# Performance work log

Hardware: AMD Instinct MI355X
Metric: run time of the kernel (lower is better)

Reference implementation:

```python
import jax, jax.numpy as jnp
import numpy as np

COORD_DIM = 2
ENTITY_DIM = 1024
FIELD_DIM = 512
INPUT_DIM = 512
NUM_ENTITIES = 512
FIELD_RESOLUTION = 10000  # grid_size = 100


def _gelu(x):
    return jax.nn.gelu(x, approximate=False)  # torch nn.GELU default (erf)


def setup_inputs() -> dict:
    key = jax.random.key(0)
    ks = jax.random.split(key, 9)
    std = 0.02  # matches _init_parameters
    B, S = 8, 4096
    x = jax.random.normal(ks[0], (B, S, INPUT_DIM), dtype=jnp.float32)
    # DensityField: density_projection = Linear(D,F) GELU Linear(F,F) GELU; coordinate_generator = Linear(F,2)
    W1 = jax.random.normal(ks[1], (INPUT_DIM, FIELD_DIM), jnp.float32) * std
    b1 = jnp.zeros((FIELD_DIM,), jnp.float32)
    W2 = jax.random.normal(ks[2], (FIELD_DIM, FIELD_DIM), jnp.float32) * std
    b2 = jnp.zeros((FIELD_DIM,), jnp.float32)
    Wc = jax.random.normal(ks[3], (FIELD_DIM, COORD_DIM), jnp.float32) * std
    bc = jnp.zeros((COORD_DIM,), jnp.float32)
    # entity_mapper: Linear(F+2, F) GELU Linear(F, E+2+1)
    We1 = jax.random.normal(ks[4], (FIELD_DIM + COORD_DIM, FIELD_DIM), jnp.float32) * std
    be1 = jnp.zeros((FIELD_DIM,), jnp.float32)
    We2 = jax.random.normal(ks[5], (FIELD_DIM, ENTITY_DIM + COORD_DIM + 1), jnp.float32) * std
    be2 = jnp.zeros((ENTITY_DIM + COORD_DIM + 1,), jnp.float32)
    # output_projection: Linear(E, 2E) GELU Linear(2E, D)
    Wo1 = jax.random.normal(ks[6], (ENTITY_DIM, 2 * ENTITY_DIM), jnp.float32) * std
    bo1 = jnp.zeros((2 * ENTITY_DIM,), jnp.float32)
    Wo2 = jax.random.normal(ks[7], (2 * ENTITY_DIM, INPUT_DIM), jnp.float32) * std
    bo2 = jnp.zeros((INPUT_DIM,), jnp.float32)
    return dict(x=x, W1=W1, b1=b1, W2=W2, b2=b2, Wc=Wc, bc=bc,
                We1=We1, be1=be1, We2=We2, be2=be2,
                Wo1=Wo1, bo1=bo1, Wo2=Wo2, bo2=bo2)


def _forward(x, W1, b1, W2, b2, Wc, bc, We1, be1, We2, be2, Wo1, bo1, Wo2, bo2):
    # --- DensityField ---
    df = _gelu(_gelu(x @ W1 + b1) @ W2 + b2)          # [B,S,F]
    coords = df @ Wc + bc                              # [B,S,2]
    # --- ContinuousEntityExtractor ---
    field_input = jnp.concatenate([coords, df], axis=-1)          # [B,S,2+F]
    ef = _gelu(field_input @ We1 + be1) @ We2 + be2                # [B,S,E+3]
    importance = jnp.linalg.norm(ef, axis=-1)                      # [B,S]
    _, top_idx = jax.lax.top_k(importance, NUM_ENTITIES)           # [B,Ne]
    sel = jnp.take_along_axis(ef, top_idx[..., None], axis=1)     # [B,Ne,E+3]
    positions = sel[..., :COORD_DIM]                               # [B,Ne,2]
    states = sel[..., COORD_DIM:COORD_DIM + ENTITY_DIM]            # [B,Ne,E]
    # --- ContinuousOutputGenerator ---
    proj = _gelu(states @ Wo1 + bo1) @ Wo2 + bo2                   # [B,Ne,D]
    grid_size = int(FIELD_RESOLUTION ** 0.5)
    g = jnp.linspace(-1.0, 1.0, grid_size)
    gx, gy = jnp.meshgrid(g, g, indexing='ij')
    grid = jnp.stack([gx.ravel(), gy.ravel()], axis=-1)            # [G2,2]
    # squared euclidean distances via expansion (torch: cdist then **2)
    g2 = jnp.sum(grid * grid, axis=-1)                             # [G2]
    p2 = jnp.sum(positions * positions, axis=-1)                   # [B,Ne]
    gp = jnp.einsum('gc,bnc->bgn', grid, positions)                # [B,G2,Ne]
    sq = g2[None, :, None] + p2[:, None, :] - 2.0 * gp             # [B,G2,Ne]
    attn = jnp.exp(-sq / 0.1)
    attn = attn / (attn.sum(axis=-1, keepdims=True) + 1e-8)
    out = jnp.einsum('bgn,bnd->bgd', attn, proj)                   # [B,G2,D]
    return out


def reference(x, W1, b1, W2, b2, Wc, bc, We1, be1, We2, be2, Wo1, bo1, Wo2, bo2):
    return _forward(x, W1, b1, W2, b2, Wc, bc, We1, be1, We2, be2, Wo1, bo1, Wo2, bo2)
```

## Files before the change

kernel.cpp:

```cpp
#include <hip/hip_runtime.h>
#include <hip/hip_bf16.h>
#include <math.h>


typedef __attribute__((ext_vector_type(8))) short bf16x8;
typedef __attribute__((ext_vector_type(4))) float f32x4;

__device__ __forceinline__ float gelu_exact(float x) {
    return 0.5f * x * (1.0f + erff(x * 0.7071067811865476f));
}

__device__ __forceinline__ void async_copy16(const void* g, void* l) {
    __builtin_amdgcn_global_load_lds(
        (const __attribute__((address_space(1))) unsigned int*)g,
        (__attribute__((address_space(3))) unsigned int*)l, 16, 0, 0);
}

__global__ __launch_bounds__(256) void split_kernel(
    const float* __restrict__ in,
    __hip_bfloat16* __restrict__ hi, __hip_bfloat16* __restrict__ lo)
{
    const int i4 = blockIdx.x * 256 + threadIdx.x;
    const float4 v = ((const float4*)in)[i4];
    __hip_bfloat16 h0 = __float2bfloat16(v.x);
    __hip_bfloat16 h1 = __float2bfloat16(v.y);
    __hip_bfloat16 h2 = __float2bfloat16(v.z);
    __hip_bfloat16 h3 = __float2bfloat16(v.w);
    __hip_bfloat16 l0 = __float2bfloat16(v.x - __bfloat162float(h0));
    __hip_bfloat16 l1 = __float2bfloat16(v.y - __bfloat162float(h1));
    __hip_bfloat16 l2 = __float2bfloat16(v.z - __bfloat162float(h2));
    __hip_bfloat16 l3 = __float2bfloat16(v.w - __bfloat162float(h3));
    union { __hip_bfloat16 h[4]; short4 s; } uh, ul;
    uh.h[0] = h0; uh.h[1] = h1; uh.h[2] = h2; uh.h[3] = h3;
    ul.h[0] = l0; ul.h[1] = l1; ul.h[2] = l2; ul.h[3] = l3;
    ((short4*)hi)[i4] = uh.s;
    ((short4*)lo)[i4] = ul.s;
}

__global__ __launch_bounds__(256) void transpose_split_kernel(
    const float* __restrict__ in,
    __hip_bfloat16* __restrict__ outH, __hip_bfloat16* __restrict__ outL,
    int K, int N)
{
    __shared__ float tile[32][33];
    const int k0 = blockIdx.y * 32, n0 = blockIdx.x * 32;
    const int t = threadIdx.x;
    const int lr = t >> 5, lc = t & 31;
    #pragma unroll
    for (int p = 0; p < 4; p++) {
        const int r = p * 8 + lr;
        const int n = n0 + lc;
        tile[r][lc] = (n < N) ? in[(size_t)(k0 + r) * N + n] : 0.f;
    }
    __syncthreads();
    #pragma unroll
    for (int p = 0; p < 4; p++) {
        const int r = p * 8 + lr;
        const float v = tile[lc][r];
        const __hip_bfloat16 h = __float2bfloat16(v);
        const __hip_bfloat16 l = __float2bfloat16(v - __bfloat162float(h));
        outH[(size_t)(n0 + r) * K + k0 + lc] = h;
        outL[(size_t)(n0 + r) * K + k0 + lc] = l;
    }
}

__global__ __launch_bounds__(256) void init_kernel(
    float* __restrict__ IMP, float* __restrict__ CRD,
    const float* __restrict__ bc)
{
    const int t = blockIdx.x * 256 + threadIdx.x;
    IMP[t] = 0.f;
    ((float2*)CRD)[t] = make_float2(bc[0], bc[1]);
}

template<bool GELU, bool RANK2, bool SPLIT, bool FUSEC, bool FUSEI>
__device__ __forceinline__ void gemm3k_body(
    const __hip_bfloat16* __restrict__ Ahi, const __hip_bfloat16* __restrict__ Alo,
    const __hip_bfloat16* __restrict__ Bhi, const __hip_bfloat16* __restrict__ Blo,
    const float* __restrict__ bias,
    float* __restrict__ Cf, int ldc,
    __hip_bfloat16* __restrict__ Chi, __hip_bfloat16* __restrict__ Clo,
    int N,
    const float* __restrict__ A2, const float* __restrict__ W2r,
    float* __restrict__ CRD, const float* __restrict__ Wc,
    float* __restrict__ IMP)
{
    __shared__ __align__(16) __hip_bfloat16 AsH[128][32];
    __shared__ __align__(16) __hip_bfloat16 AsL[128][32];
    __shared__ __align__(16) __hip_bfloat16 BsH[128][32];
    __shared__ __align__(16) __hip_bfloat16 BsL[128][32];
    const int t = threadIdx.x;
    const int wave = t >> 6, lane = t & 63;
    const int wave_m = wave >> 1, wave_n = wave & 1;
    const int fr = lane & 15, quad = lane >> 4;
    const int m0 = blockIdx.y * 128;
    const int n0 = blockIdx.x * 128;
    const int srow = lane >> 2;
    const int skc  = (lane & 3) * 8;

    f32x4 acc[4][4] = {};

    for (int k0 = 0; k0 < 512; k0 += 32) {
        #pragma unroll
        for (int s = 0; s < 2; s++) {
            const int seg = wave * 2 + s;
            const int row = seg * 16 + srow;
            const size_t ao = (size_t)(m0 + row) * 512 + k0 + skc;
            const size_t bo = (size_t)(n0 + row) * 512 + k0 + skc;
            async_copy16(Ahi + ao, &AsH[seg * 16][0]);
            async_copy16(Alo + ao, &AsL[seg * 16][0]);
            async_copy16(Bhi + bo, &BsH[seg * 16][0]);
            async_copy16(Blo + bo, &BsL[seg * 16][0]);
        }
        __syncthreads();
        bf16x8 ah[4], al[4], bh[4], bl[4];
        #pragma unroll
        for (int i = 0; i < 4; i++) {
            ah[i] = *(const bf16x8*)&AsH[wave_m * 64 + i * 16 + fr][quad * 8];
            al[i] = *(const bf16x8*)&AsL[wave_m * 64 + i * 16 + fr][quad * 8];
        }
        #pragma unroll
        for (int j = 0; j < 4; j++) {
            bh[j] = *(const bf16x8*)&BsH[wave_n * 64 + j * 16 + fr][quad * 8];
            bl[j] = *(const bf16x8*)&BsL[wave_n * 64 + j * 16 + fr][quad * 8];
        }
        #pragma unroll
        for (int i = 0; i < 4; i++)
            #pragma unroll
            for (int j = 0; j < 4; j++)
                acc[i][j] = __builtin_amdgcn_mfma_f32_16x16x32_bf16(
                    ah[i], bh[j], acc[i][j], 0, 0, 0);
        #pragma unroll
        for (int i = 0; i < 4; i++)
            #pragma unroll
            for (int j = 0; j < 4; j++)
                acc[i][j] = __builtin_amdgcn_mfma_f32_16x16x32_bf16(
                    ah[i], bl[j], acc[i][j], 0, 0, 0);
        #pragma unroll
        for (int i = 0; i < 4; i++)
            #pragma unroll
            for (int j = 0; j < 4; j++)
                acc[i][j] = __builtin_amdgcn_mfma_f32_16x16x32_bf16(
                    al[i], bh[j], acc[i][j], 0, 0, 0);
        __syncthreads();
    }

    #pragma unroll
    for (int i = 0; i < 4; i++) {
        const int gmb = m0 + wave_m * 64 + i * 16 + quad * 4;
        float a2x[4], a2y[4];
        if (RANK2) {
            #pragma unroll
            for (int r = 0; r < 4; r++) {
                a2x[r] = A2[(size_t)(gmb + r) * 2];
                a2y[r] = A2[(size_t)(gmb + r) * 2 + 1];
            }
        }
        float f0[4] = {0.f, 0.f, 0.f, 0.f};
        float f1[4] = {0.f, 0.f, 0.f, 0.f};
        #pragma unroll
        for (int j = 0; j < 4; j++) {
            const int gn = n0 + wave_n * 64 + j * 16 + fr;
            const bool nok = SPLIT || (gn < N);
            const float bv = nok ? bias[gn] : 0.f;
            float w2a = 0.f, w2b = 0.f;
            if (RANK2) { w2a = W2r[gn]; w2b = W2r[512 + gn]; }
            float wcx = 0.f, wcy = 0.f;
            if (FUSEC) {
                const float2 wc = ((const float2*)Wc)[gn];
                wcx = wc.x; wcy = wc.y;
            }
            #pragma unroll
            for (int r = 0; r < 4; r++) {
                const int gm = gmb + r;
                float v = acc[i][j][r] + bv;
                if (RANK2) v += a2x[r] * w2a + a2y[r] * w2b;
                if (GELU) v = gelu_exact(v);
                if (SPLIT) {
                    const __hip_bfloat16 h = __float2bfloat16(v);
                    const __hip_bfloat16 l =
                        __float2bfloat16(v - __bfloat162float(h));
                    Chi[(size_t)gm * 512 + gn] = h;
                    Clo[(size_t)gm * 512 + gn] = l;
                } else if (nok) {
                    Cf[(size_t)gm * ldc + gn] = v;
                }
                if (FUSEC) { f0[r] += v * wcx; f1[r] += v * wcy; }
                if (FUSEI && nok) f0[r] += v * v;
            }
        }
        if (FUSEC || FUSEI) {
            #pragma unroll
            for (int r = 0; r < 4; r++) {
                float a = f0[r], b = f1[r];
                #pragma unroll
                for (int off = 1; off < 16; off <<= 1) {
                    a += __shfl_xor(a, off);
                    if (FUSEC) b += __shfl_xor(b, off);
                }
                if (fr == 0) {
                    if (FUSEC) {
                        atomicAdd(&CRD[(size_t)(gmb + r) * 2],     a);
                        atomicAdd(&CRD[(size_t)(gmb + r) * 2 + 1], b);
                    } else {
                        atomicAdd(&IMP[gmb + r], a);
                    }
                }
            }
        }
    }
}

__global__ __launch_bounds__(256) void gemm_h1(
    const __hip_bfloat16* __restrict__ Ahi, const __hip_bfloat16* __restrict__ Alo,
    const __hip_bfloat16* __restrict__ Bhi, const __hip_bfloat16* __restrict__ Blo,
    const float* __restrict__ bias,
    __hip_bfloat16* __restrict__ Chi, __hip_bfloat16* __restrict__ Clo)
{
    gemm3k_body<true, false, true, false, false>(
        Ahi, Alo, Bhi, Blo, bias, nullptr, 0, Chi, Clo, 512,
        nullptr, nullptr, nullptr, nullptr, nullptr);
}

__global__ __launch_bounds__(256) void gemm_df(
    const __hip_bfloat16* __restrict__ Ahi, const __hip_bfloat16* __restrict__ Alo,
    const __hip_bfloat16* __restrict__ Bhi, const __hip_bfloat16* __restrict__ Blo,
    const float* __restrict__ bias,
    __hip_bfloat16* __restrict__ Chi, __hip_bfloat16* __restrict__ Clo,
    float* __restrict__ CRD, const float* __restrict__ Wc)
{
    gemm3k_body<true, false, true, true, false>(
        Ahi, Alo, Bhi, Blo, bias, nullptr, 0, Chi, Clo, 512,
        nullptr, nullptr, CRD, Wc, nullptr);
}

__global__ __launch_bounds__(256) void gemm_h3(
    const __hip_bfloat16* __restrict__ Ahi, const __hip_bfloat16* __restrict__ Alo,
    const __hip_bfloat16* __restrict__ Bhi, const __hip_bfloat16* __restrict__ Blo,
    const float* __restrict__ bias,
    __hip_bfloat16* __restrict__ Chi, __hip_bfloat16* __restrict__ Clo,
    const float* __restrict__ A2, const float* __restrict__ W2r)
{
    gemm3k_body<true, true, true, false, false>(
        Ahi, Alo, Bhi, Blo, bias, nullptr, 0, Chi, Clo, 512,
        A2, W2r, nullptr, nullptr, nullptr);
}

__global__ __launch_bounds__(256) void gemm_ef(
    const __hip_bfloat16* __restrict__ Ahi, const __hip_bfloat16* __restrict__ Alo,
    const __hip_bfloat16* __restrict__ Bhi, const __hip_bfloat16* __restrict__ Blo,
    const float* __restrict__ bias,
    float* __restrict__ Cf, float* __restrict__ IMP)
{
    gemm3k_body<false, false, false, false, true>(
        Ahi, Alo, Bhi, Blo, bias, Cf, 1027, nullptr, nullptr, 1027,
        nullptr, nullptr, nullptr, nullptr, IMP);
}

__global__ __launch_bounds__(1024) void topk_kernel(
    const float* __restrict__ IMP, int* __restrict__ IDX)
{
    __shared__ float v[4096];
    __shared__ int   ix[4096];
    const int b = blockIdx.x, t = threadIdx.x;
    for (int i = t; i < 4096; i += 1024) {
        v[i] = sqrtf(IMP[b * 4096 + i]);
        ix[i] = i;
    }
    __syncthreads();
    for (int k = 2; k <= 4096; k <<= 1) {
        for (int j = k >> 1; j > 0; j >>= 1) {
            for (int q = 0; q < 4; q++) {
                const int i = t + (q << 10);
                const int l = i ^ j;
                if (l > i) {
                    const float vi = v[i], vl = v[l];
                    const int   ii = ix[i], il = ix[l];
                    const bool after = (vi < vl) || (vi == vl && ii > il);
                    const bool dirAsc = ((i & k) == 0);
                    if (dirAsc ? after : !after) {
                        v[i] = vl; v[l] = vi; ix[i] = il; ix[l] = ii;
                    }
                }
            }
            __syncthreads();
        }
    }
    if (t < 512) IDX[b * 512 + t] = ix[t];
}

__global__ __launch_bounds__(256) void gather_kernel(
    const float* __restrict__ EF, const int* __restrict__ IDX,
    float* __restrict__ POS, __hip_bfloat16* __restrict__ ST)
{
    const int bn  = blockIdx.x;
    const int b   = bn >> 9;
    const int row = IDX[bn];
    const float* src = EF + ((size_t)(b * 4096) + row) * 1027;
    const int t = threadIdx.x;
    if (t < 2) POS[(size_t)bn * 2 + t] = src[t];
    __hip_bfloat16* dst = ST + (size_t)bn * 1024;
    for (int k = t; k < 1024; k += 256) dst[k] = __float2bfloat16(src[2 + k]);
}

__global__ __launch_bounds__(256) void transpose_cvt_kernel(
    const float* __restrict__ in, __hip_bfloat16* __restrict__ out,
    int K, int N)
{
    __shared__ float tile[32][33];
    const int k0 = blockIdx.y * 32, n0 = blockIdx.x * 32;
    const int t = threadIdx.x;
    const int lr = t >> 5, lc = t & 31;
    #pragma unroll
    for (int p = 0; p < 4; p++) {
        const int r = p * 8 + lr;
        tile[r][lc] = in[(size_t)(k0 + r) * N + n0 + lc];
    }
    __syncthreads();
    #pragma unroll
    for (int p = 0; p < 4; p++) {
        const int r = p * 8 + lr;
        out[(size_t)(n0 + r) * K + k0 + lc] = __float2bfloat16(tile[lc][r]);
    }
}

__global__ __launch_bounds__(256) void transpose_proj_kernel(
    const __hip_bfloat16* __restrict__ in, __hip_bfloat16* __restrict__ out)
{
    __shared__ __hip_bfloat16 tile[32][33];
    const int b = blockIdx.z;
    const int n0 = blockIdx.y * 32, d0 = blockIdx.x * 32;
    const int t = threadIdx.x;
    const int lr = t >> 5, lc = t & 31;
    #pragma unroll
    for (int p = 0; p < 4; p++) {
        const int r = p * 8 + lr;
        tile[r][lc] = in[((size_t)b * 512 + n0 + r) * 512 + d0 + lc];
    }
    __syncthreads();
    #pragma unroll
    for (int p = 0; p < 4; p++) {
        const int r = p * 8 + lr;
        out[((size_t)b * 512 + d0 + r) * 512 + n0 + lc] = tile[lc][r];
    }
}

template<bool GELU>
__device__ __forceinline__ void gemm_post_body(
    const __hip_bfloat16* __restrict__ A,
    const __hip_bfloat16* __restrict__ BT,
    const float* __restrict__ bias,
    __hip_bfloat16* __restrict__ C,
    int N, int K)
{
    __shared__ __align__(16) __hip_bfloat16 As[2][128][32];
    __shared__ __align__(16) __hip_bfloat16 Bs[2][128][32];
    const int t = threadIdx.x;
    const int wave = t >> 6, lane = t & 63;
    const int wave_m = wave >> 1, wave_n = wave & 1;
    const int fr = lane & 15, quad = lane >> 4;
    const int gx = gridDim.x;
    const int nwg = gx * gridDim.y;
    int lid = blockIdx.y * gx + blockIdx.x;
    {
        const int chunk = nwg >> 3;
        lid = (lid & 7) * chunk + (lid >> 3);
    }
    const int m0 = (lid / gx) * 128;
    const int n0 = (lid % gx) * 128;
    const int srow = lane >> 2;
    const int skc  = (lane & 3) * 8;
    const int nsteps = K >> 5;

    f32x4 acc[4][4] = {};

    auto STAGE = [&](int buf, int step) {
        const int kk = step << 5;
        #pragma unroll
        for (int s = 0; s < 2; s++) {
            const int seg = wave * 2 + s;
            const int row = seg * 16 + srow;
            async_copy16(A  + (size_t)(m0 + row) * K + kk + skc,
                         &As[buf][seg * 16][0]);
            async_copy16(BT + (size_t)(n0 + row) * K + kk + skc,
                         &Bs[buf][seg * 16][0]);
        }
    };

    STAGE(0, 0);
    __syncthreads();
    int cur = 0;
    for (int step = 0; step < nsteps; ++step) {
        if (step + 1 < nsteps) STAGE(cur ^ 1, step + 1);
        bf16x8 af[4], bfv[4];
        #pragma unroll
        for (int i = 0; i < 4; i++)
            af[i] = *(const bf16x8*)&As[cur][wave_m * 64 + i * 16 + fr][quad * 8];
        #pragma unroll
        for (int j = 0; j < 4; j++)
            bfv[j] = *(const bf16x8*)&Bs[cur][wave_n * 64 + j * 16 + fr][quad * 8];
        #pragma unroll
        for (int i = 0; i < 4; i++)
            #pragma unroll
            for (int j = 0; j < 4; j++)
                acc[i][j] = __builtin_amdgcn_mfma_f32_16x16x32_bf16(
                    af[i], bfv[j], acc[i][j], 0, 0, 0);
        __syncthreads();
        cur ^= 1;
    }
    #pragma unroll
    for (int i = 0; i < 4; i++) {
        const int gm = m0 + wave_m * 64 + i * 16 + quad * 4;
        #pragma unroll
        for (int j = 0; j < 4; j++) {
            const int gn = n0 + wave_n * 64 + j * 16 + fr;
            const float bv = bias[gn];
            #pragma unroll
            for (int r = 0; r < 4; r++) {
                float v = acc[i][j][r] + bv;
                if (GELU) v = gelu_exact(v);
                C[(size_t)(gm + r) * N + gn] = __float2bfloat16(v);
            }
        }
    }
}

__global__ __launch_bounds__(256, 4) void gemm_o1(
    const __hip_bfloat16* __restrict__ A, const __hip_bfloat16* __restrict__ BT,
    const float* __restrict__ bias, __hip_bfloat16* __restrict__ C,
    int N, int K)
{
    gemm_post_body<true>(A, BT, bias, C, N, K);
}

__global__ __launch_bounds__(256, 4) void gemm_o2(
    const __hip_bfloat16* __restrict__ A, const __hip_bfloat16* __restrict__ BT,
    const float* __restrict__ bias, __hip_bfloat16* __restrict__ C,
    int N, int K)
{
    gemm_post_body<false>(A, BT, bias, C, N, K);
}

__global__ __launch_bounds__(256) void attn_mfma_kernel(
    const float* __restrict__ POS,
    const __hip_bfloat16* __restrict__ PROJT,
    float* __restrict__ OUT)
{
    __shared__ __align__(16) __hip_bfloat16 Bs[256][32];
    __shared__ float2 pos_s[512];
    __shared__ float srow_s[4][16];
    const int t = threadIdx.x;
    const int wave = t >> 6, lane = t & 63;
    const int fr = lane & 15, quad = lane >> 4;
    const int b  = blockIdx.z;
    const int g0 = blockIdx.x * 64;
    const int d0 = blockIdx.y * 256;

    {
        const float2* p = (const float2*)(POS + (size_t)b * 512 * 2);
        pos_s[t]       = p[t];
        pos_s[256 + t] = p[256 + t];
    }
    const int g = g0 + wave * 16 + fr;
    const bool gv = g < 10000;
    const float step = 2.0f / 99.0f;
    const int gi = gv ? (g / 100) : 0;
    const int gj = gv ? (g - gi * 100) : 0;
    const float gx = -1.f + step * (float)gi;
    const float gy = -1.f + step * (float)gj;

    f32x4 acc[16] = {};
    float wsum = 0.f;
    __syncthreads();

    for (int n0 = 0; n0 < 512; n0 += 32) {
        #pragma unroll
        for (int s = 0; s < 4; s++) {
            const int seg = wave * 4 + s;
            const __hip_bfloat16* gB = PROJT
                + ((size_t)b * 512 + d0 + seg * 16 + (lane >> 2)) * 512
                + n0 + (lane & 3) * 8;
            async_copy16(gB, &Bs[seg * 16][0]);
        }
        bf16x8 wf;
        float wl = 0.f;
        #pragma unroll
        for (int j = 0; j < 8; j++) {
            const int n = n0 + quad * 8 + j;
            const float2 pn = pos_s[n];
            const float dx = gx - pn.x, dy = gy - pn.y;
            const float w = gv ? __expf(-10.0f * (dx * dx + dy * dy)) : 0.f;
            const __hip_bfloat16 wb = __float2bfloat16(w);
            union { __hip_bfloat16 h; short s; } u; u.h = wb;
            wf[j] = u.s;
            wl += __bfloat162float(wb);
        }
        wsum += wl;
        __syncthreads();
        #pragma unroll
        for (int j = 0; j < 16; j++) {
            const bf16x8 bv = *(const bf16x8*)&Bs[j * 16 + fr][quad * 8];
            acc[j] = __builtin_amdgcn_mfma_f32_16x16x32_bf16(wf, bv, acc[j], 0, 0, 0);
        }
        __syncthreads();
    }
    wsum += __shfl_xor(wsum, 16);
    wsum += __shfl_xor(wsum, 32);
    if (lane < 16) srow_s[wave][lane] = wsum;
    __syncthreads();
    const int rbase = quad * 4;
    float inv[4];
    #pragma unroll
    for (int r = 0; r < 4; r++)
        inv[r] = 1.0f / (srow_s[wave][rbase + r] + 1e-8f);
    #pragma unroll
    for (int j = 0; j < 16; j++) {
        const int col = d0 + j * 16 + fr;
        #pragma unroll
        for (int r = 0; r < 4; r++) {
            const int gr = g0 + wave * 16 + rbase + r;
            if (gr < 10000)
                OUT[((size_t)b * 10000 + gr) * 512 + col] = acc[j][r] * inv[r];
        }
    }
}

extern "C" void kernel_launch(void* const* d_in, const int* in_sizes, int n_in,
                              void* d_out, int out_size, void* d_ws, size_t ws_size,
                              hipStream_t stream)
{
    const float* x   = (const float*)d_in[0];
    const float* W1  = (const float*)d_in[1];
    const float* b1  = (const float*)d_in[2];
    const float* W2  = (const float*)d_in[3];
    const float* b2  = (const float*)d_in[4];
    const float* Wc  = (const float*)d_in[5];
    const float* bc  = (const float*)d_in[6];
    const float* We1 = (const float*)d_in[7];
    const float* be1 = (const float*)d_in[8];
    const float* We2 = (const float*)d_in[9];
    const float* be2 = (const float*)d_in[10];
    const float* Wo1 = (const float*)d_in[11];
    const float* bo1 = (const float*)d_in[12];
    const float* Wo2 = (const float*)d_in[13];
    const float* bo2 = (const float*)d_in[14];
    float* out = (float*)d_out;

    const size_t BS = 32768;
    const size_t ACT = BS * 512;
    __hip_bfloat16* P0h = (__hip_bfloat16*)d_ws;
    __hip_bfloat16* P0l = P0h + ACT;
    __hip_bfloat16* P1h = P0l + ACT;
    __hip_bfloat16* P1l = P1h + ACT;
    float* EF  = (float*)(P1l + ACT);
    float* CRD = EF + BS * 1027;
    float* IMP = CRD + BS * 2;
    int*   IDX = (int*)(IMP + BS);
    float* POS = (float*)(IDX + 4096);
    __hip_bfloat16* W1Th = (__hip_bfloat16*)(POS + 4096 * 2);
    __hip_bfloat16* W1Tl = W1Th + 512 * 512;
    __hip_bfloat16* W2Th = W1Tl + 512 * 512;
    __hip_bfloat16* W2Tl = W2Th + 512 * 512;
    __hip_bfloat16* We1Th = W2Tl + 512 * 512;
    __hip_bfloat16* We1Tl = We1Th + 512 * 512;
    __hip_bfloat16* We2Th = We1Tl + 512 * 512;
    __hip_bfloat16* We2Tl = We2Th + (size_t)1152 * 512;
    __hip_bfloat16* ST    = P0h;
    __hip_bfloat16* H4    = ST + (size_t)4096 * 1024;
    __hip_bfloat16* PROJ  = H4 + (size_t)4096 * 2048;
    __hip_bfloat16* PROJT = PROJ + (size_t)4096 * 512;
    __hip_bfloat16* Wo1T  = PROJT + (size_t)4096 * 512;
    __hip_bfloat16* Wo2T  = Wo1T + (size_t)2048 * 1024;

    dim3 blk(256);
    split_kernel<<<dim3(16384), blk, 0, stream>>>(x, P0h, P0l);
    transpose_split_kernel<<<dim3(16, 16), blk, 0, stream>>>(W1, W1Th, W1Tl, 512, 512);
    transpose_split_kernel<<<dim3(16, 16), blk, 0, stream>>>(W2, W2Th, W2Tl, 512, 512);
    transpose_split_kernel<<<dim3(16, 16), blk, 0, stream>>>(We1 + 2 * 512, We1Th, We1Tl, 512, 512);
    transpose_split_kernel<<<dim3(36, 16), blk, 0, stream>>>(We2, We2Th, We2Tl, 512, 1027);
    init_kernel<<<dim3(128), blk, 0, stream>>>(IMP, CRD, bc);
    gemm_h1<<<dim3(4, 256), blk, 0, stream>>>(
        P0h, P0l, W1Th, W1Tl, b1, P1h, P1l);
    gemm_df<<<dim3(4, 256), blk, 0, stream>>>(
        P1h, P1l, W2Th, W2Tl, b2, P0h, P0l, CRD, Wc);
    gemm_h3<<<dim3(4, 256), blk, 0, stream>>>(
        P0h, P0l, We1Th, We1Tl, be1, P1h, P1l, CRD, We1);
    gemm_ef<<<dim3(9, 256), blk, 0, stream>>>(
        P1h, P1l, We2Th, We2Tl, be2, EF, IMP);
    topk_kernel<<<dim3(8), dim3(1024), 0, stream>>>(IMP, IDX);
    transpose_cvt_kernel<<<dim3(64, 32), blk, 0, stream>>>(Wo1, Wo1T, 1024, 2048);
    transpose_cvt_kernel<<<dim3(16, 64), blk, 0, stream>>>(Wo2, Wo2T, 2048, 512);
    gather_kernel<<<dim3(4096), blk, 0, stream>>>(EF, IDX, POS, ST);
    gemm_o1<<<dim3(16, 32), blk, 0, stream>>>(ST, Wo1T, bo1, H4, 2048, 1024);
    gemm_o2<<<dim3(4, 32), blk, 0, stream>>>(H4, Wo2T, bo2, PROJ, 512, 2048);
    transpose_proj_kernel<<<dim3(16, 16, 8), blk, 0, stream>>>(PROJ, PROJT);
    attn_mfma_kernel<<<dim3(157, 2, 8), blk, 0, stream>>>(POS, PROJT, out);
}
```

Measured before the change: 925.2 us.

## Unfuse coord/importance reductions from GEMMs and remap blocks per XCD

Removes the atomic-based coordinate and importance reductions from the GEMM epilogues and computes them in separate row-reduction kernels instead. This drops the init kernel and the atomics, and makes the coordinate and importance sums deterministic. The GEMM block index is also remapped so that consecutive M-chunks are grouped per XCD, which is meant to improve L2 reuse. The cost is two extra kernel launches and an extra pass over the DF and EF buffers (EF is large, about 4096×8×1027 floats).

```diff
diff --git a/kernel.cpp b/kernel.cpp
--- a/kernel.cpp
+++ b/kernel.cpp
@@ -64,16 +64,7 @@
     }
 }
 
-__global__ __launch_bounds__(256) void init_kernel(
-    float* __restrict__ IMP, float* __restrict__ CRD,
-    const float* __restrict__ bc)
-{
-    const int t = blockIdx.x * 256 + threadIdx.x;
-    IMP[t] = 0.f;
-    ((float2*)CRD)[t] = make_float2(bc[0], bc[1]);
-}
-
-template<bool GELU, bool RANK2, bool SPLIT, bool FUSEC, bool FUSEI>
+template<bool GELU, bool RANK2, bool SPLIT, bool BOUNDS>
 __device__ __forceinline__ void gemm3k_body(
     const __hip_bfloat16* __restrict__ Ahi, const __hip_bfloat16* __restrict__ Alo,
     const __hip_bfloat16* __restrict__ Bhi, const __hip_bfloat16* __restrict__ Blo,
@@ -81,9 +72,7 @@
     float* __restrict__ Cf, int ldc,
     __hip_bfloat16* __restrict__ Chi, __hip_bfloat16* __restrict__ Clo,
     int N,
-    const float* __restrict__ A2, const float* __restrict__ W2r,
-    float* __restrict__ CRD, const float* __restrict__ Wc,
-    float* __restrict__ IMP)
+    const float* __restrict__ A2, const float* __restrict__ W2r)
 {
     __shared__ __align__(16) __hip_bfloat16 AsH[128][32];
     __shared__ __align__(16) __hip_bfloat16 AsL[128][32];
@@ -93,8 +82,12 @@
     const int wave = t >> 6, lane = t & 63;
     const int wave_m = wave >> 1, wave_n = wave & 1;
     const int fr = lane & 15, quad = lane >> 4;
-    const int m0 = blockIdx.y * 128;
-    const int n0 = blockIdx.x * 128;
+    const int gx = gridDim.x;
+    const int L = blockIdx.y * gx + blockIdx.x;
+    const int xcd = L & 7, rem = L >> 3;
+    const int mchunk = gridDim.y >> 3;
+    const int m0 = (xcd * mchunk + rem / gx) * 128;
+    const int n0 = (rem % gx) * 128;
     const int srow = lane >> 2;
     const int skc  = (lane & 3) * 8;
 
@@ -148,33 +141,19 @@
     #pragma unroll
     for (int i = 0; i < 4; i++) {
         const int gmb = m0 + wave_m * 64 + i * 16 + quad * 4;
-        float a2x[4], a2y[4];
-        if (RANK2) {
-            #pragma unroll
-            for (int r = 0; r < 4; r++) {
-                a2x[r] = A2[(size_t)(gmb + r) * 2];
-                a2y[r] = A2[(size_t)(gmb + r) * 2 + 1];
-            }
-        }
-        float f0[4] = {0.f, 0.f, 0.f, 0.f};
-        float f1[4] = {0.f, 0.f, 0.f, 0.f};
         #pragma unroll
         for (int j = 0; j < 4; j++) {
             const int gn = n0 + wave_n * 64 + j * 16 + fr;
-            const bool nok = SPLIT || (gn < N);
+            const bool nok = !BOUNDS || (gn < N);
             const float bv = nok ? bias[gn] : 0.f;
             float w2a = 0.f, w2b = 0.f;
             if (RANK2) { w2a = W2r[gn]; w2b = W2r[512 + gn]; }
-            float wcx = 0.f, wcy = 0.f;
-            if (FUSEC) {
-                const float2 wc = ((const float2*)Wc)[gn];
-                wcx = wc.x; wcy = wc.y;
-            }
             #pragma unroll
             for (int r = 0; r < 4; r++) {
                 const int gm = gmb + r;
                 float v = acc[i][j][r] + bv;
-                if (RANK2) v += a2x[r] * w2a + a2y[r] * w2b;
+                if (RANK2)
+                    v += A2[(size_t)gm * 2] * w2a + A2[(size_t)gm * 2 + 1] * w2b;
                 if (GELU) v = gelu_exact(v);
                 if (SPLIT) {
                     const __hip_bfloat16 h = __float2bfloat16(v);
@@ -185,27 +164,6 @@
                 } else if (nok) {
                     Cf[(size_t)gm * ldc + gn] = v;
                 }
-                if (FUSEC) { f0[r] += v * wcx; f1[r] += v * wcy; }
-                if (FUSEI && nok) f0[r] += v * v;
-            }
-        }
-        if (FUSEC || FUSEI) {
-            #pragma unroll
-            for (int r = 0; r < 4; r++) {
-                float a = f0[r], b = f1[r];
-                #pragma unroll
-                for (int off = 1; off < 16; off <<= 1) {
-                    a += __shfl_xor(a, off);
-                    if (FUSEC) b += __shfl_xor(b, off);
-                }
-                if (fr == 0) {
-                    if (FUSEC) {
-                        atomicAdd(&CRD[(size_t)(gmb + r) * 2],     a);
-                        atomicAdd(&CRD[(size_t)(gmb + r) * 2 + 1], b);
-                    } else {
-                        atomicAdd(&IMP[gmb + r], a);
-                    }
-                }
             }
         }
     }
@@ -217,21 +175,18 @@
     const float* __restrict__ bias,
     __hip_bfloat16* __restrict__ Chi, __hip_bfloat16* __restrict__ Clo)
 {
-    gemm3k_body<true, false, true, false, false>(
-        Ahi, Alo, Bhi, Blo, bias, nullptr, 0, Chi, Clo, 512,
-        nullptr, nullptr, nullptr, nullptr, nullptr);
+    gemm3k_body<true, false, true, false>(
+        Ahi, Alo, Bhi, Blo, bias, nullptr, 0, Chi, Clo, 512, nullptr, nullptr);
 }
 
 __global__ __launch_bounds__(256) void gemm_df(
     const __hip_bfloat16* __restrict__ Ahi, const __hip_bfloat16* __restrict__ Alo,
     const __hip_bfloat16* __restrict__ Bhi, const __hip_bfloat16* __restrict__ Blo,
     const float* __restrict__ bias,
-    __hip_bfloat16* __restrict__ Chi, __hip_bfloat16* __restrict__ Clo,
-    float* __restrict__ CRD, const float* __restrict__ Wc)
-{
-    gemm3k_body<true, false, true, true, false>(
-        Ahi, Alo, Bhi, Blo, bias, nullptr, 0, Chi, Clo, 512,
-        nullptr, nullptr, CRD, Wc, nullptr);
+    __hip_bfloat16* __restrict__ Chi, __hip_bfloat16* __restrict__ Clo)
+{
+    gemm3k_body<true, false, true, false>(
+        Ahi, Alo, Bhi, Blo, bias, nullptr, 0, Chi, Clo, 512, nullptr, nullptr);
 }
 
 __global__ __launch_bounds__(256) void gemm_h3(
@@ -241,20 +196,61 @@
     __hip_bfloat16* __restrict__ Chi, __hip_bfloat16* __restrict__ Clo,
     const float* __restrict__ A2, const float* __restrict__ W2r)
 {
-    gemm3k_body<true, true, true, false, false>(
-        Ahi, Alo, Bhi, Blo, bias, nullptr, 0, Chi, Clo, 512,
-        A2, W2r, nullptr, nullptr, nullptr);
+    gemm3k_body<true, true, true, false>(
+        Ahi, Alo, Bhi, Blo, bias, nullptr, 0, Chi, Clo, 512, A2, W2r);
 }
 
 __global__ __launch_bounds__(256) void gemm_ef(
     const __hip_bfloat16* __restrict__ Ahi, const __hip_bfloat16* __restrict__ Alo,
     const __hip_bfloat16* __restrict__ Bhi, const __hip_bfloat16* __restrict__ Blo,
     const float* __restrict__ bias,
-    float* __restrict__ Cf, float* __restrict__ IMP)
-{
-    gemm3k_body<false, false, false, false, true>(
+    float* __restrict__ Cf)
+{
+    gemm3k_body<false, false, false, true>(
         Ahi, Alo, Bhi, Blo, bias, Cf, 1027, nullptr, nullptr, 1027,
-        nullptr, nullptr, nullptr, nullptr, IMP);
+        nullptr, nullptr);
+}
+
+__global__ __launch_bounds__(256) void coords_kernel(
+    const __hip_bfloat16* __restrict__ DFh, const __hip_bfloat16* __restrict__ DFl,
+    const float* __restrict__ Wc,
+    const float* __restrict__ bc, float* __restrict__ CRD)
+{
+    const int gid  = blockIdx.x * 256 + threadIdx.x;
+    const int row  = gid >> 6;
+    const int lane = gid & 63;
+    const __hip_bfloat16* dh = DFh + (size_t)row * 512;
+    const __hip_bfloat16* dl = DFl + (size_t)row * 512;
+    float s0 = 0.f, s1 = 0.f;
+    for (int k = lane; k < 512; k += 64) {
+        const float v = __bfloat162float(dh[k]) + __bfloat162float(dl[k]);
+        const float2 wc = ((const float2*)Wc)[k];
+        s0 += v * wc.x;
+        s1 += v * wc.y;
+    }
+    #pragma unroll
+    for (int off = 32; off; off >>= 1) {
+        s0 += __shfl_down(s0, off);
+        s1 += __shfl_down(s1, off);
+    }
+    if (lane == 0) {
+        CRD[(size_t)row * 2 + 0] = s0 + bc[0];
+        CRD[(size_t)row * 2 + 1] = s1 + bc[1];
+    }
+}
+
+__global__ __launch_bounds__(256) void importance_kernel(
+    const float* __restrict__ EF, float* __restrict__ IMP)
+{
+    const int gid  = blockIdx.x * 256 + threadIdx.x;
+    const int row  = gid >> 6;
+    const int lane = gid & 63;
+    const float* e = EF + (size_t)row * 1027;
+    float ss = 0.f;
+    for (int k = lane; k < 1027; k += 64) { const float v = e[k]; ss += v * v; }
+    #pragma unroll
+    for (int off = 32; off; off >>= 1) ss += __shfl_down(ss, off);
+    if (lane == 0) IMP[row] = sqrtf(ss);
 }
 
 __global__ __launch_bounds__(1024) void topk_kernel(
@@ -263,10 +259,7 @@
     __shared__ float v[4096];
     __shared__ int   ix[4096];
     const int b = blockIdx.x, t = threadIdx.x;
-    for (int i = t; i < 4096; i += 1024) {
-        v[i] = sqrtf(IMP[b * 4096 + i]);
-        ix[i] = i;
-    }
+    for (int i = t; i < 4096; i += 1024) { v[i] = IMP[b * 4096 + i]; ix[i] = i; }
     __syncthreads();
     for (int k = 2; k <= 4096; k <<= 1) {
         for (int j = k >> 1; j > 0; j >>= 1) {
@@ -578,15 +571,16 @@
     transpose_split_kernel<<<dim3(16, 16), blk, 0, stream>>>(W2, W2Th, W2Tl, 512, 512);
     transpose_split_kernel<<<dim3(16, 16), blk, 0, stream>>>(We1 + 2 * 512, We1Th, We1Tl, 512, 512);
     transpose_split_kernel<<<dim3(36, 16), blk, 0, stream>>>(We2, We2Th, We2Tl, 512, 1027);
-    init_kernel<<<dim3(128), blk, 0, stream>>>(IMP, CRD, bc);
     gemm_h1<<<dim3(4, 256), blk, 0, stream>>>(
         P0h, P0l, W1Th, W1Tl, b1, P1h, P1l);
     gemm_df<<<dim3(4, 256), blk, 0, stream>>>(
-        P1h, P1l, W2Th, W2Tl, b2, P0h, P0l, CRD, Wc);
+        P1h, P1l, W2Th, W2Tl, b2, P0h, P0l);
+    coords_kernel<<<dim3(8192), blk, 0, stream>>>(P0h, P0l, Wc, bc, CRD);
     gemm_h3<<<dim3(4, 256), blk, 0, stream>>>(
         P0h, P0l, We1Th, We1Tl, be1, P1h, P1l, CRD, We1);
     gemm_ef<<<dim3(9, 256), blk, 0, stream>>>(
-        P1h, P1l, We2Th, We2Tl, be2, EF, IMP);
+        P1h, P1l, We2Th, We2Tl, be2, EF);
+    importance_kernel<<<dim3(8192), blk, 0, stream>>>(EF, IMP);
     topk_kernel<<<dim3(8), dim3(1024), 0, stream>>>(IMP, IDX);
     transpose_cvt_kernel<<<dim3(64, 32), blk, 0, stream>>>(Wo1, Wo1T, 1024, 2048);
     transpose_cvt_kernel<<<dim3(16, 64), blk, 0, stream>>>(Wo2, Wo2T, 2048, 512);
```

Measured after the change: 899.3 us. 2.8% less time.
